# Optimization experiments

Hardware: AMD Instinct MI355X
Metric: run time of the kernel (lower is better)

The kernel has to match this reference:

```python
import jax, jax.numpy as jnp
import numpy as np

B = 16384      # batch
N = 128        # number of DNPU nodes (experts)
I = 3          # data electrodes per node
C = 4          # control electrodes per node
E = I + C      # total electrodes = 7
H = 90         # surrogate-model hidden width
L = 3          # number of extra hidden layers


def setup_inputs() -> dict:
    key = jax.random.key(0)
    ks = jax.random.split(key, 8)
    s_in = 1.0 / np.sqrt(E)
    s_h = 1.0 / np.sqrt(H)
    return {
        "x": jax.random.normal(ks[0], (B, N * I), dtype=jnp.float32),
        "controls": jax.random.uniform(ks[1], (N, C), dtype=jnp.float32, minval=-1.2, maxval=0.6),
        "W_in": jax.random.normal(ks[2], (N, E, H), dtype=jnp.float32) * s_in,
        "b_in": jax.random.normal(ks[3], (N, H), dtype=jnp.float32) * 0.1,
        "W_hid": jax.random.normal(ks[4], (L, N, H, H), dtype=jnp.float32) * s_h,
        "b_hid": jax.random.normal(ks[5], (L, N, H), dtype=jnp.float32) * 0.1,
        "W_out": jax.random.normal(ks[6], (N, H), dtype=jnp.float32) * s_h,
        "b_out": jax.random.normal(ks[7], (N,), dtype=jnp.float32) * 0.1,
    }


def reference(x, controls, W_in, b_in, W_hid, b_hid, W_out, b_out):
    # DNPU_Layer: partition x into N chunks of I, each node merges its data
    # electrodes with its learned control voltages into a 7-electrode vector,
    # evaluates the shared surrogate MLP with per-node parameters, outputs 1
    # current per node; results are concatenated along dim 1 -> [B, N].
    b = x.shape[0]
    xd = x.reshape(b, N, I)                                   # partition_input
    ctrl = jnp.broadcast_to(controls[None], (b, N, C))        # per-node controls
    e = jnp.concatenate([xd, ctrl], axis=-1)                  # [B, N, E]
    h = jax.nn.relu(jnp.einsum('bne,neh->bnh', e, W_in) + b_in)
    for l in range(L):  # fixed small layer count
        h = jax.nn.relu(jnp.einsum('bnh,nhk->bnk', h, W_hid[l]) + b_hid[l])
    out = jnp.einsum('bnh,nh->bn', h, W_out) + b_out          # [B, N]
    return out
```

## Files before the change

### kernel.cpp

```cpp
#include <hip/hip_runtime.h>
#include <stdint.h>

namespace {
constexpr int kB  = 16384;
constexpr int kN  = 128;
constexpr int kI  = 3;
constexpr int kC  = 4;
constexpr int kH  = 90;
constexpr int kL  = 3;
constexpr int KP  = 96;
constexpr int FB_PER_NODE = 57;
constexpr int NODE_USH    = FB_PER_NODE * 512;
constexpr size_t WT_BYTES = (size_t)kN * NODE_USH * 2;
constexpr size_t WO_OFF   = WT_BYTES;
constexpr size_t XK_OFF   = WO_OFF + (size_t)kN * KP * 4;
}

typedef __attribute__((ext_vector_type(8))) short bf16x8;
typedef __attribute__((ext_vector_type(16))) float f32x16;

__device__ __forceinline__ uint32_t pack_bf16(float lo, float hi) {
#if __has_builtin(__builtin_amdgcn_cvt_pk_bf16_f32)
  auto r = __builtin_amdgcn_cvt_pk_bf16_f32(lo, hi);
  union { decltype(r) v; uint32_t u; } c; c.v = r; return c.u;
#else
  union { float f; uint32_t i; } a, b; a.f = lo; b.f = hi;
  uint32_t ua = a.i + 0x8000u;
  uint32_t ub = b.i + 0x8000u;
  return __builtin_amdgcn_perm(ub, ua, 0x07060302);
#endif
}
__device__ __forceinline__ ushort f2bf(float f) {
  union { float f; uint32_t i; } v; v.f = f;
  uint32_t u = v.i + 0x7FFFu + ((v.i >> 16) & 1u);
  return (ushort)(u >> 16);
}

__device__ __forceinline__ void pl32swap(uint32_t& a, uint32_t& b) {
#if __has_builtin(__builtin_amdgcn_permlane32_swap)
  auto r = __builtin_amdgcn_permlane32_swap(a, b, false, false);
  a = (uint32_t)r[0]; b = (uint32_t)r[1];
#else
  uint32_t sa = (uint32_t)__shfl_xor((int)a, 32);
  uint32_t sb = (uint32_t)__shfl_xor((int)b, 32);
  bool lo = (threadIdx.x & 63) < 32;
  uint32_t na = lo ? a : sb;
  uint32_t nb = lo ? sa : b;
  a = na; b = nb;
#endif
}

__device__ __forceinline__ void stage16(const ushort* g, ushort* l) {
  __builtin_amdgcn_global_load_lds(
      (const __attribute__((address_space(1))) void*)g,
      (__attribute__((address_space(3))) void*)l, 16, 0, 0);
}

__global__ __launch_bounds__(256) void prep_kernel(
    const float* __restrict__ x,
    const float* __restrict__ W_in, const float* __restrict__ b_in,
    const float* __restrict__ W_hid, const float* __restrict__ b_hid,
    const float* __restrict__ W_out, const float* __restrict__ b_out,
    ushort* __restrict__ wt, float* __restrict__ wo, ushort* __restrict__ xk)
{
  __shared__ float smem[kH * (kH + 1) + kH];
  const int tid = threadIdx.x;
  const int bid = blockIdx.x;

  if (bid < 4 * kN) {
    float* ldsw = smem;
    float* ldsb = smem + kH * (kH + 1);
    const int node  = bid & (kN - 1);
    const int layer = bid >> 7;
    const int ksrc  = (layer == 0) ? (kI + kC) : kH;
    const float* src;
    const float* bsrc;
    if (layer == 0) { src = W_in + (size_t)node * (kI + kC) * kH; bsrc = b_in + (size_t)node * kH; }
    else {
      int l = layer - 1;
      src  = W_hid + (size_t)(l * kN + node) * kH * kH;
      bsrc = b_hid + (size_t)(l * kN + node) * kH;
    }
    for (int idx = tid; idx < ksrc * kH; idx += 256)
      ldsw[(idx / kH) * (kH + 1) + (idx % kH)] = src[idx];
    if (tid < kH) ldsb[tid] = bsrc[tid];
    __syncthreads();
    ushort* dstbase = wt + (size_t)node * NODE_USH
                    + (size_t)((layer == 0) ? 0 : 3 + (layer - 1) * 18) * 512;
    const int nch = (layer == 0) ? 192 : 1152;
#pragma unroll
    for (int it = 0; it < 5; ++it) {
      int c = tid + it * 256;
      if (c < nch) {
        int fb = c >> 6, lane = c & 63;
        int ks = (layer == 0) ? 0 : fb / 3;
        int mt = (layer == 0) ? fb : fb % 3;
        int j  = mt * 32 + (lane & 31);
        int kb = ks * 16 + (lane >> 5) * 8;
        float v[8];
#pragma unroll
        for (int i = 0; i < 8; ++i) {
          int k = kb + i;
          float t = 0.f;
          if (j < kH) {
            if (k < ksrc)       t = ldsw[k * (kH + 1) + j];
            else if (k == ksrc) t = ldsb[j];
          }
          v[i] = t;
        }
        uint4 p;
        p.x = pack_bf16(v[0], v[1]); p.y = pack_bf16(v[2], v[3]);
        p.z = pack_bf16(v[4], v[5]); p.w = pack_bf16(v[6], v[7]);
        *(uint4*)&dstbase[(size_t)c * 8] = p;
      }
    }
  } else if (bid < 4 * kN + 4) {
    int base = (bid - 4 * kN) * 3072;
    for (int t = 0; t < 12; ++t) {
      int idx = base + t * 256 + tid;
      int node = idx / KP, j = idx % KP;
      float v = 0.f;
      if (j < kH)       v = W_out[node * kH + j];
      else if (j == kH) v = b_out[node];
      wo[idx] = v;
    }
  } else {
    int xb = bid - (4 * kN + 4);
    int b0 = (xb & 255) * 64;
    int c0 = (xb >> 8) * 96;
    float* lds = smem;
    for (int idx = tid; idx < 64 * 96; idx += 256) {
      int r = idx / 96, c = idx % 96;
      lds[r * 97 + c] = x[(size_t)(b0 + r) * (kN * kI) + c0 + c];
    }
    __syncthreads();
#pragma unroll
    for (int it = 0; it < 3; ++it) {
      int c = tid + it * 256;
      int nk = c >> 3, b = (c & 7) * 8;
      float v[8];
#pragma unroll
      for (int i = 0; i < 8; ++i) v[i] = lds[(b + i) * 97 + nk];
      uint4 p;
      p.x = pack_bf16(v[0], v[1]); p.y = pack_bf16(v[2], v[3]);
      p.z = pack_bf16(v[4], v[5]); p.w = pack_bf16(v[6], v[7]);
      *(uint4*)&xk[(size_t)(c0 + nk) * kB + b0 + b] = p;
    }
  }
}

__global__ __launch_bounds__(256, 3) void dnpu_kernel(
    const ushort* __restrict__ xk, const float* __restrict__ controls,
    const ushort* __restrict__ wt, const float* __restrict__ wo,
    float* __restrict__ out)
{
  __shared__ __align__(16) ushort wbuf[2][18 * 512];

  const int tid  = threadIdx.x;
  const int lane = tid & 63;
  const int wid  = tid >> 6;
  const int node = (int)(blockIdx.x & 127);
  const int m0   = (int)(blockIdx.x >> 7) * 256 + wid * 64;
  const int col  = lane & 31;
  const int hh   = lane >> 5;

  const ushort* wnode = wt + (size_t)node * NODE_USH;

  auto stage_hid = [&](int l, ushort* buf) {
    const ushort* src = wnode + (size_t)(3 + l * 18) * 512;
#pragma unroll
    for (int r = 0; r < 4; ++r)
      stage16(src + (size_t)(r * 256 + wid * 64 + lane) * 8,
              buf + (size_t)(r * 256 + wid * 64) * 8);
    if (wid < 2)
      stage16(src + (size_t)(1024 + wid * 64 + lane) * 8,
              buf + (size_t)(1024 + wid * 64) * 8);
  };

  if (wid < 3)
    stage16(wnode + (size_t)(wid * 64 + lane) * 8, &wbuf[0][(size_t)(wid * 64) * 8]);
  stage_hid(0, &wbuf[1][0]);

  const f32x16 zf = (f32x16)0.0f;

  bf16x8 b0[2];
  {
    const ushort cb0 = f2bf(controls[node * kC + 0]);
    const ushort cb1 = f2bf(controls[node * kC + 1]);
    const ushort cb2 = f2bf(controls[node * kC + 2]);
    const ushort cb3 = f2bf(controls[node * kC + 3]);
    const ushort* xp = xk + (size_t)node * kI * kB + m0 + col;
#pragma unroll
    for (int nt = 0; nt < 2; ++nt) {
      union { ushort s[8]; bf16x8 v; } f;
      f.s[0] = xp[0 * kB + nt * 32];
      f.s[1] = xp[1 * kB + nt * 32];
      f.s[2] = xp[2 * kB + nt * 32];
      f.s[3] = cb0; f.s[4] = cb1; f.s[5] = cb2; f.s[6] = cb3;
      f.s[7] = 0x3F80;
      bf16x8 z = (bf16x8){0,0,0,0,0,0,0,0};
      if (hh) b0[nt] = z; else b0[nt] = f.v;
    }
  }

  union BF { uint32_t u[4]; bf16x8 v; };
  BF Bc[6][2], Bn[6][2];

  auto pack_mt = [&](int mt, const f32x16& a0, const f32x16& a1, BF (&Bout)[6][2]) {
#pragma unroll
    for (int nt = 0; nt < 2; ++nt) {
      const f32x16& a = nt ? a1 : a0;
      float v[16];
#pragma unroll
      for (int r = 0; r < 16; ++r) v[r] = fmaxf(a[r], 0.f);
      if (mt == 2) v[14] = (hh == 0) ? 1.0f : v[14];
      uint32_t P[8];
#pragma unroll
      for (int w = 0; w < 8; ++w) P[w] = pack_bf16(v[2 * w], v[2 * w + 1]);
      uint32_t q0 = P[0], q2 = P[2]; pl32swap(q0, q2);
      uint32_t q1 = P[1], q3 = P[3]; pl32swap(q1, q3);
      uint32_t q4 = P[4], q6 = P[6]; pl32swap(q4, q6);
      uint32_t q5 = P[5], q7 = P[7]; pl32swap(q5, q7);
      Bout[2 * mt][nt].u[0] = q0; Bout[2 * mt][nt].u[1] = q1;
      Bout[2 * mt][nt].u[2] = q2; Bout[2 * mt][nt].u[3] = q3;
      Bout[2 * mt + 1][nt].u[0] = q4; Bout[2 * mt + 1][nt].u[1] = q5;
      Bout[2 * mt + 1][nt].u[2] = q6; Bout[2 * mt + 1][nt].u[3] = q7;
    }
  };

  auto hidden = [&](const ushort* buf, BF (&Bin)[6][2], BF (&Bout)[6][2]) {
#pragma unroll
    for (int mt = 0; mt < 3; ++mt) {
      f32x16 a0, a1;
      __builtin_amdgcn_s_setprio(1);
#pragma unroll
      for (int ks = 0; ks < 6; ++ks) {
        bf16x8 afr = *(const bf16x8*)&buf[(size_t)(ks * 3 + mt) * 512 + lane * 8];
        a0 = __builtin_amdgcn_mfma_f32_32x32x16_bf16(afr, Bin[ks][0].v,
                                                     ks ? a0 : zf, 0, 0, 0);
        a1 = __builtin_amdgcn_mfma_f32_32x32x16_bf16(afr, Bin[ks][1].v,
                                                     ks ? a1 : zf, 0, 0, 0);
      }
      __builtin_amdgcn_s_setprio(0);
      pack_mt(mt, a0, a1, Bout);
    }
  };

  __syncthreads();

  {
#pragma unroll
    for (int mt = 0; mt < 3; ++mt) {
      bf16x8 afr = *(const bf16x8*)&wbuf[0][(size_t)mt * 512 + lane * 8];
      __builtin_amdgcn_s_setprio(1);
      f32x16 a0 = __builtin_amdgcn_mfma_f32_32x32x16_bf16(afr, b0[0], zf, 0, 0, 0);
      f32x16 a1 = __builtin_amdgcn_mfma_f32_32x32x16_bf16(afr, b0[1], zf, 0, 0, 0);
      __builtin_amdgcn_s_setprio(0);
      pack_mt(mt, a0, a1, Bc);
    }
  }

  __syncthreads();
  stage_hid(1, &wbuf[0][0]);
  hidden(&wbuf[1][0], Bc, Bn);

  __syncthreads();
  stage_hid(2, &wbuf[1][0]);
  hidden(&wbuf[0][0], Bn, Bc);

  __syncthreads();

  {
    const float* wop = wo + node * KP;
    float s0 = 0.f, s1 = 0.f;
#pragma unroll
    for (int mt = 0; mt < 3; ++mt) {
      f32x16 a0, a1;
      __builtin_amdgcn_s_setprio(1);
#pragma unroll
      for (int ks = 0; ks < 6; ++ks) {
        bf16x8 afr = *(const bf16x8*)&wbuf[1][(size_t)(ks * 3 + mt) * 512 + lane * 8];
        a0 = __builtin_amdgcn_mfma_f32_32x32x16_bf16(afr, Bc[ks][0].v,
                                                     ks ? a0 : zf, 0, 0, 0);
        a1 = __builtin_amdgcn_mfma_f32_32x32x16_bf16(afr, Bc[ks][1].v,
                                                     ks ? a1 : zf, 0, 0, 0);
      }
      __builtin_amdgcn_s_setprio(0);
#pragma unroll
      for (int g = 0; g < 4; ++g) {
        float4 wf = *(const float4*)&wop[mt * 32 + g * 8 + hh * 4];
#pragma unroll
        for (int r2 = 0; r2 < 4; ++r2) {
          int r = g * 4 + r2;
          float w = (r2 == 0) ? wf.x : (r2 == 1) ? wf.y : (r2 == 2) ? wf.z : wf.w;
          float h0v = fmaxf(a0[r], 0.f);
          float h1v = fmaxf(a1[r], 0.f);
          if (mt == 2 && r == 14) {
            h0v = (hh == 0) ? 1.0f : h0v;
            h1v = (hh == 0) ? 1.0f : h1v;
          }
          s0 += h0v * w; s1 += h1v * w;
        }
      }
    }
    s0 += __shfl_xor(s0, 32);
    s1 += __shfl_xor(s1, 32);
    float r = hh ? s1 : s0;
    out[(size_t)(m0 + lane) * kN + node] = r;
  }
}

extern "C" void kernel_launch(void* const* d_in, const int* in_sizes, int n_in,
                              void* d_out, int out_size, void* d_ws, size_t ws_size,
                              hipStream_t stream) {
  const float* x        = (const float*)d_in[0];
  const float* controls = (const float*)d_in[1];
  const float* W_in     = (const float*)d_in[2];
  const float* b_in     = (const float*)d_in[3];
  const float* W_hid    = (const float*)d_in[4];
  const float* b_hid    = (const float*)d_in[5];
  const float* W_out    = (const float*)d_in[6];
  const float* b_out    = (const float*)d_in[7];
  float* out = (float*)d_out;

  ushort* wt = (ushort*)d_ws;
  float*  wo = (float*)((char*)d_ws + WO_OFF);
  ushort* xk = (ushort*)((char*)d_ws + XK_OFF);

  hipLaunchKernelGGL(prep_kernel, dim3(4 * kN + 4 + 1024), dim3(256), 0, stream,
                     x, W_in, b_in, W_hid, b_hid, W_out, b_out, wt, wo, xk);

  dim3 grid((kB / 256) * kN);
  hipLaunchKernelGGL(dnpu_kernel, grid, dim3(256), 0, stream,
                     xk, controls, wt, wo, out);
}
```

Before: 225.3 us.

## Halve per-wave batch tile and split K accumulation into two chains

Each wave now processes 32 batch rows instead of 64, so the grid doubles and the per-thread B-fragment and accumulator arrays shrink by half. Launch bounds are raised to 4 waves-per-EU to use the freed registers for higher occupancy. To keep two independent MFMA chains in flight, the K loop is split into even and odd accumulators that are summed before the ReLU. The tradeoff is that each block reloads the node's weights into LDS for half as many rows, doubling weight staging traffic, and half the lanes idle on the final store.

```diff
diff --git a/kernel.cpp b/kernel.cpp
--- a/kernel.cpp
+++ b/kernel.cpp
@@ -149,7 +149,7 @@
   }
 }
 
-__global__ __launch_bounds__(256, 3) void dnpu_kernel(
+__global__ __launch_bounds__(256, 4) void dnpu_kernel(
     const ushort* __restrict__ xk, const float* __restrict__ controls,
     const ushort* __restrict__ wt, const float* __restrict__ wo,
     float* __restrict__ out)
@@ -160,7 +160,7 @@
   const int lane = tid & 63;
   const int wid  = tid >> 6;
   const int node = (int)(blockIdx.x & 127);
-  const int m0   = (int)(blockIdx.x >> 7) * 256 + wid * 64;
+  const int m0   = (int)(blockIdx.x >> 7) * 128 + wid * 32;
   const int col  = lane & 31;
   const int hh   = lane >> 5;
 
@@ -183,66 +183,60 @@
 
   const f32x16 zf = (f32x16)0.0f;
 
-  bf16x8 b0[2];
+  bf16x8 b0;
   {
     const ushort cb0 = f2bf(controls[node * kC + 0]);
     const ushort cb1 = f2bf(controls[node * kC + 1]);
     const ushort cb2 = f2bf(controls[node * kC + 2]);
     const ushort cb3 = f2bf(controls[node * kC + 3]);
     const ushort* xp = xk + (size_t)node * kI * kB + m0 + col;
-#pragma unroll
-    for (int nt = 0; nt < 2; ++nt) {
-      union { ushort s[8]; bf16x8 v; } f;
-      f.s[0] = xp[0 * kB + nt * 32];
-      f.s[1] = xp[1 * kB + nt * 32];
-      f.s[2] = xp[2 * kB + nt * 32];
-      f.s[3] = cb0; f.s[4] = cb1; f.s[5] = cb2; f.s[6] = cb3;
-      f.s[7] = 0x3F80;
-      bf16x8 z = (bf16x8){0,0,0,0,0,0,0,0};
-      if (hh) b0[nt] = z; else b0[nt] = f.v;
-    }
+    union { ushort s[8]; bf16x8 v; } f;
+    f.s[0] = xp[0 * kB];
+    f.s[1] = xp[1 * kB];
+    f.s[2] = xp[2 * kB];
+    f.s[3] = cb0; f.s[4] = cb1; f.s[5] = cb2; f.s[6] = cb3;
+    f.s[7] = 0x3F80;
+    bf16x8 z = (bf16x8){0,0,0,0,0,0,0,0};
+    b0 = hh ? z : f.v;
   }
 
   union BF { uint32_t u[4]; bf16x8 v; };
-  BF Bc[6][2], Bn[6][2];
-
-  auto pack_mt = [&](int mt, const f32x16& a0, const f32x16& a1, BF (&Bout)[6][2]) {
-#pragma unroll
-    for (int nt = 0; nt < 2; ++nt) {
-      const f32x16& a = nt ? a1 : a0;
-      float v[16];
-#pragma unroll
-      for (int r = 0; r < 16; ++r) v[r] = fmaxf(a[r], 0.f);
-      if (mt == 2) v[14] = (hh == 0) ? 1.0f : v[14];
-      uint32_t P[8];
-#pragma unroll
-      for (int w = 0; w < 8; ++w) P[w] = pack_bf16(v[2 * w], v[2 * w + 1]);
-      uint32_t q0 = P[0], q2 = P[2]; pl32swap(q0, q2);
-      uint32_t q1 = P[1], q3 = P[3]; pl32swap(q1, q3);
-      uint32_t q4 = P[4], q6 = P[6]; pl32swap(q4, q6);
-      uint32_t q5 = P[5], q7 = P[7]; pl32swap(q5, q7);
-      Bout[2 * mt][nt].u[0] = q0; Bout[2 * mt][nt].u[1] = q1;
-      Bout[2 * mt][nt].u[2] = q2; Bout[2 * mt][nt].u[3] = q3;
-      Bout[2 * mt + 1][nt].u[0] = q4; Bout[2 * mt + 1][nt].u[1] = q5;
-      Bout[2 * mt + 1][nt].u[2] = q6; Bout[2 * mt + 1][nt].u[3] = q7;
-    }
+  BF Bc[6], Bn[6];
+
+  auto pack_mt = [&](int mt, const f32x16& ae, const f32x16& ao, BF* Bout) {
+    float v[16];
+#pragma unroll
+    for (int r = 0; r < 16; ++r) v[r] = fmaxf(ae[r] + ao[r], 0.f);
+    if (mt == 2) v[14] = (hh == 0) ? 1.0f : v[14];
+    uint32_t P[8];
+#pragma unroll
+    for (int w = 0; w < 8; ++w) P[w] = pack_bf16(v[2 * w], v[2 * w + 1]);
+    uint32_t q0 = P[0], q2 = P[2]; pl32swap(q0, q2);
+    uint32_t q1 = P[1], q3 = P[3]; pl32swap(q1, q3);
+    uint32_t q4 = P[4], q6 = P[6]; pl32swap(q4, q6);
+    uint32_t q5 = P[5], q7 = P[7]; pl32swap(q5, q7);
+    Bout[2 * mt].u[0] = q0; Bout[2 * mt].u[1] = q1;
+    Bout[2 * mt].u[2] = q2; Bout[2 * mt].u[3] = q3;
+    Bout[2 * mt + 1].u[0] = q4; Bout[2 * mt + 1].u[1] = q5;
+    Bout[2 * mt + 1].u[2] = q6; Bout[2 * mt + 1].u[3] = q7;
   };
 
-  auto hidden = [&](const ushort* buf, BF (&Bin)[6][2], BF (&Bout)[6][2]) {
+  auto hidden = [&](const ushort* buf, BF* Bin, BF* Bout) {
 #pragma unroll
     for (int mt = 0; mt < 3; ++mt) {
-      f32x16 a0, a1;
+      f32x16 ae, ao;
       __builtin_amdgcn_s_setprio(1);
 #pragma unroll
-      for (int ks = 0; ks < 6; ++ks) {
-        bf16x8 afr = *(const bf16x8*)&buf[(size_t)(ks * 3 + mt) * 512 + lane * 8];
-        a0 = __builtin_amdgcn_mfma_f32_32x32x16_bf16(afr, Bin[ks][0].v,
-                                                     ks ? a0 : zf, 0, 0, 0);
-        a1 = __builtin_amdgcn_mfma_f32_32x32x16_bf16(afr, Bin[ks][1].v,
-                                                     ks ? a1 : zf, 0, 0, 0);
+      for (int kp = 0; kp < 3; ++kp) {
+        bf16x8 af0 = *(const bf16x8*)&buf[(size_t)((2 * kp) * 3 + mt) * 512 + lane * 8];
+        bf16x8 af1 = *(const bf16x8*)&buf[(size_t)((2 * kp + 1) * 3 + mt) * 512 + lane * 8];
+        ae = __builtin_amdgcn_mfma_f32_32x32x16_bf16(af0, Bin[2 * kp].v,
+                                                     kp ? ae : zf, 0, 0, 0);
+        ao = __builtin_amdgcn_mfma_f32_32x32x16_bf16(af1, Bin[2 * kp + 1].v,
+                                                     kp ? ao : zf, 0, 0, 0);
       }
       __builtin_amdgcn_s_setprio(0);
-      pack_mt(mt, a0, a1, Bout);
+      pack_mt(mt, ae, ao, Bout);
     }
   };
 
@@ -253,10 +247,9 @@
     for (int mt = 0; mt < 3; ++mt) {
       bf16x8 afr = *(const bf16x8*)&wbuf[0][(size_t)mt * 512 + lane * 8];
       __builtin_amdgcn_s_setprio(1);
-      f32x16 a0 = __builtin_amdgcn_mfma_f32_32x32x16_bf16(afr, b0[0], zf, 0, 0, 0);
-      f32x16 a1 = __builtin_amdgcn_mfma_f32_32x32x16_bf16(afr, b0[1], zf, 0, 0, 0);
+      f32x16 a0 = __builtin_amdgcn_mfma_f32_32x32x16_bf16(afr, b0, zf, 0, 0, 0);
       __builtin_amdgcn_s_setprio(0);
-      pack_mt(mt, a0, a1, Bc);
+      pack_mt(mt, a0, zf, Bc);
     }
   }
 
@@ -272,18 +265,19 @@
 
   {
     const float* wop = wo + node * KP;
-    float s0 = 0.f, s1 = 0.f;
+    float s0 = 0.f;
 #pragma unroll
     for (int mt = 0; mt < 3; ++mt) {
-      f32x16 a0, a1;
+      f32x16 ae, ao;
       __builtin_amdgcn_s_setprio(1);
 #pragma unroll
-      for (int ks = 0; ks < 6; ++ks) {
-        bf16x8 afr = *(const bf16x8*)&wbuf[1][(size_t)(ks * 3 + mt) * 512 + lane * 8];
-        a0 = __builtin_amdgcn_mfma_f32_32x32x16_bf16(afr, Bc[ks][0].v,
-                                                     ks ? a0 : zf, 0, 0, 0);
-        a1 = __builtin_amdgcn_mfma_f32_32x32x16_bf16(afr, Bc[ks][1].v,
-                                                     ks ? a1 : zf, 0, 0, 0);
+      for (int kp = 0; kp < 3; ++kp) {
+        bf16x8 af0 = *(const bf16x8*)&wbuf[1][(size_t)((2 * kp) * 3 + mt) * 512 + lane * 8];
+        bf16x8 af1 = *(const bf16x8*)&wbuf[1][(size_t)((2 * kp + 1) * 3 + mt) * 512 + lane * 8];
+        ae = __builtin_amdgcn_mfma_f32_32x32x16_bf16(af0, Bc[2 * kp].v,
+                                                     kp ? ae : zf, 0, 0, 0);
+        ao = __builtin_amdgcn_mfma_f32_32x32x16_bf16(af1, Bc[2 * kp + 1].v,
+                                                     kp ? ao : zf, 0, 0, 0);
       }
       __builtin_amdgcn_s_setprio(0);
 #pragma unroll
@@ -293,20 +287,16 @@
         for (int r2 = 0; r2 < 4; ++r2) {
           int r = g * 4 + r2;
           float w = (r2 == 0) ? wf.x : (r2 == 1) ? wf.y : (r2 == 2) ? wf.z : wf.w;
-          float h0v = fmaxf(a0[r], 0.f);
-          float h1v = fmaxf(a1[r], 0.f);
-          if (mt == 2 && r == 14) {
-            h0v = (hh == 0) ? 1.0f : h0v;
-            h1v = (hh == 0) ? 1.0f : h1v;
-          }
-          s0 += h0v * w; s1 += h1v * w;
+          float hv = fmaxf(ae[r] + ao[r], 0.f);
+          if (mt == 2 && r == 14)
+            hv = (hh == 0) ? 1.0f : hv;
+          s0 += hv * w;
         }
       }
     }
     s0 += __shfl_xor(s0, 32);
-    s1 += __shfl_xor(s1, 32);
-    float r = hh ? s1 : s0;
-    out[(size_t)(m0 + lane) * kN + node] = r;
+    if (hh == 0)
+      out[(size_t)(m0 + col) * kN + node] = s0;
   }
 }
 
@@ -330,7 +320,7 @@
   hipLaunchKernelGGL(prep_kernel, dim3(4 * kN + 4 + 1024), dim3(256), 0, stream,
                      x, W_in, b_in, W_hid, b_hid, W_out, b_out, wt, wo, xk);
 
-  dim3 grid((kB / 256) * kN);
+  dim3 grid((kB / 128) * kN);
   hipLaunchKernelGGL(dnpu_kernel, grid, dim3(256), 0, stream,
                      xk, controls, wt, wo, out);
 }
```

Measured after the change: 224.4 us. Within noise of the previous version (-0.4%).
